# Performance work log

Hardware: AMD Instinct MI355X
Metric: run time of the kernel (lower is better)

Reference implementation:

```python
import jax, jax.numpy as jnp
import numpy as np
import math

NUM_HEADS = 16
ATTN_WIDTH = 256


def setup_inputs() -> dict:
    key = jax.random.key(0)
    ks = jax.random.split(key, 5)
    B, S, C, H = 2, 2048, 1024, 1024
    scale = 0.02
    return {
        "x": jax.random.normal(ks[0], (B, S, C), dtype=jnp.float32),
        "Wq": jax.random.normal(ks[1], (C, H), dtype=jnp.float32) * scale,
        "Wk": jax.random.normal(ks[2], (C, H), dtype=jnp.float32) * scale,
        "Wv": jax.random.normal(ks[3], (C, H), dtype=jnp.float32) * scale,
        "Wo": jax.random.normal(ks[4], (H, C), dtype=jnp.float32) * scale,
    }


def reference(x, Wq, Wk, Wv, Wo):
    B, S, C = x.shape
    H = NUM_HEADS
    dh = Wq.shape[1] // H  # head dim; Q.size(-1) in torch code

    def split_heads(t):
        # [B, S, H*dh] -> [B, H, S, dh]
        return t.reshape(B, S, H, dh).transpose(0, 2, 1, 3)

    q = split_heads(x @ Wq)
    k = split_heads(x @ Wk)
    v = split_heads(x @ Wv)

    scores = jnp.einsum("bhqd,bhkd->bhqk", q, k) / math.sqrt(dh)
    # exp-shift (first 'softmax-like' step, unnormalized)
    scores = jnp.exp(scores - jnp.max(scores, axis=-1, keepdims=True))
    # banded mask: tril(attn_width//2 - 1).triu(-(attn_width//2))
    i = jnp.arange(S)[:, None]
    j = jnp.arange(S)[None, :]
    d = j - i
    half = ATTN_WIDTH // 2
    mask = (d <= half - 1) & (d >= -half)
    scores = jnp.where(mask, scores, 0.0)
    # second softmax over the masked exp-scores (zeros contribute exp(0)=1)
    weights = jax.nn.softmax(scores, axis=-1)

    out = jnp.einsum("bhqk,bhkd->bhqd", weights, v)  # [B, H, S, dh]
    out = out.transpose(0, 2, 1, 3).reshape(B, S, H * dh)
    return out @ Wo
```

## Files before the change

### kernel.cpp

```cpp
#include <hip/hip_runtime.h>
#include <math.h>

typedef __bf16 bf16_t;
typedef bf16_t bf16x8 __attribute__((ext_vector_type(8)));
typedef bf16_t bf16x4 __attribute__((ext_vector_type(4)));
typedef float f32x4 __attribute__((ext_vector_type(4)));

constexpr int S_ = 2048;
constexpr float SCALE = 0.125f;

#define MFMA_B16(a, b, c) __builtin_amdgcn_mfma_f32_16x16x32_bf16(a, b, c, 0, 0, 0)

#define WAIT_VM0()   __builtin_amdgcn_s_waitcnt(0x0F70)
#define WAIT_LGKM0() __builtin_amdgcn_s_waitcnt(0xC07F)
#define BARRIER()    __builtin_amdgcn_s_barrier()

typedef __attribute__((address_space(1))) const void* as1_cvp;
typedef __attribute__((address_space(3))) void* as3_vp;

__device__ __forceinline__ void gl2lds16(const void* g, void* l)
{
    __builtin_amdgcn_global_load_lds((as1_cvp)g, (as3_vp)l, 16, 0, 0);
}

__global__ __launch_bounds__(256) void prep(const float* __restrict__ x,
                                            const float* __restrict__ Wq,
                                            const float* __restrict__ Wk,
                                            const float* __restrict__ Wv,
                                            const float* __restrict__ Wo,
                                            bf16_t* __restrict__ xb,
                                            bf16_t* __restrict__ Wqt,
                                            bf16_t* __restrict__ Wkt,
                                            bf16_t* __restrict__ Wvt,
                                            bf16_t* __restrict__ Wot,
                                            float* __restrict__ vsp)
{
    __shared__ float T[64][65];
    const int blk = blockIdx.x;
    const int tid = threadIdx.x;
    if (blk < 1024) {
#pragma unroll
        for (int u = 0; u < 4; ++u) {
            const int g = blk * 1024 + u * 256 + tid;
            const float4 v = ((const float4*)x)[g];
            bf16x4 o;
            o[0] = (bf16_t)v.x; o[1] = (bf16_t)v.y;
            o[2] = (bf16_t)v.z; o[3] = (bf16_t)v.w;
            *(bf16x4*)&xb[(size_t)g * 4] = o;
        }
    } else if (blk < 2048) {
        const int rem = blk - 1024;
        const int wsel = rem >> 8, t = rem & 255;
        const float* src = (wsel == 0) ? Wq : (wsel == 1) ? Wk : (wsel == 2) ? Wv : Wo;
        bf16_t* dst = (wsel == 0) ? Wqt : (wsel == 1) ? Wkt : (wsel == 2) ? Wvt : Wot;
        const int k0 = (t >> 4) * 64, n0 = (t & 15) * 64;
        const int rr = tid >> 4, c4 = (tid & 15) * 4;
#pragma unroll
        for (int u = 0; u < 4; ++u) {
            const float4 v = *(const float4*)&src[(size_t)(k0 + u * 16 + rr) * 1024 + n0 + c4];
            T[u * 16 + rr][c4 + 0] = v.x; T[u * 16 + rr][c4 + 1] = v.y;
            T[u * 16 + rr][c4 + 2] = v.z; T[u * 16 + rr][c4 + 3] = v.w;
        }
        __syncthreads();
#pragma unroll
        for (int u = 0; u < 4; ++u) {
            bf16x4 o;
#pragma unroll
            for (int e = 0; e < 4; ++e) o[e] = (bf16_t)T[c4 + e][u * 16 + rr];
            *(bf16x4*)&dst[(size_t)(n0 + u * 16 + rr) * 1024 + k0 + c4] = o;
        }
    } else {
#pragma unroll
        for (int u = 0; u < 8; ++u) vsp[u * 256 + tid] = 0.f;
    }
}

template <int MODE>
__device__ __forceinline__ void mfma_gemm_body(const bf16_t* __restrict__ A,
                                               const bf16_t* __restrict__ Bt,
                                               void* __restrict__ dst,
                                               float* __restrict__ vsum_out,
                                               int m0, int n0)
{
    __shared__ bf16_t As[8192];
    __shared__ bf16_t Bs[8192];

    const int tid = threadIdx.x;
    const int lane = tid & 63, wid = tid >> 6;
    const int l15 = lane & 15, quad = lane >> 4;
    const int wm = (wid & 1) * 64, wn = (wid >> 1) * 64;

    const int srow = wid * 32 + (lane >> 2);
    const int scg8 = (lane & 3) * 8;
    const bf16_t* Ag0 = A  + (size_t)(m0 + srow) * 1024 + scg8;
    const bf16_t* Ag1 = A  + (size_t)(m0 + srow + 16) * 1024 + scg8;
    const bf16_t* Bg0 = Bt + (size_t)(n0 + srow) * 1024 + scg8;
    const bf16_t* Bg1 = Bt + (size_t)(n0 + srow + 16) * 1024 + scg8;

    f32x4 acc[4][4];
#pragma unroll
    for (int i = 0; i < 4; ++i)
#pragma unroll
        for (int j = 0; j < 4; ++j) acc[i][j] = (f32x4){0.f, 0.f, 0.f, 0.f};

    gl2lds16(Ag0, As + (wid * 2 + 0) * 512);
    gl2lds16(Ag1, As + (wid * 2 + 1) * 512);
    gl2lds16(Bg0, Bs + (wid * 2 + 0) * 512);
    gl2lds16(Bg1, Bs + (wid * 2 + 1) * 512);

    for (int it = 0; it < 32; ++it) {
        WAIT_VM0();
        BARRIER();
        const int cur = it & 1, nxt = cur ^ 1;
        if (it + 1 < 32) {
            const int k0 = (it + 1) * 32;
            gl2lds16(Ag0 + k0, As + nxt * 4096 + (wid * 2 + 0) * 512);
            gl2lds16(Ag1 + k0, As + nxt * 4096 + (wid * 2 + 1) * 512);
            gl2lds16(Bg0 + k0, Bs + nxt * 4096 + (wid * 2 + 0) * 512);
            gl2lds16(Bg1 + k0, Bs + nxt * 4096 + (wid * 2 + 1) * 512);
        }
        bf16x8 af[4], bfr[4];
#pragma unroll
        for (int mt = 0; mt < 4; ++mt)
            af[mt] = *(const bf16x8*)&As[cur * 4096 + (wm + mt * 16 + l15) * 32 + quad * 8];
#pragma unroll
        for (int nt = 0; nt < 4; ++nt)
            bfr[nt] = *(const bf16x8*)&Bs[cur * 4096 + (wn + nt * 16 + l15) * 32 + quad * 8];
#pragma unroll
        for (int mt = 0; mt < 4; ++mt)
#pragma unroll
            for (int nt = 0; nt < 4; ++nt)
                acc[mt][nt] = MFMA_B16(bfr[nt], af[mt], acc[mt][nt]);
    }

#pragma unroll
    for (int mt = 0; mt < 4; ++mt) {
        const int m = m0 + wm + mt * 16 + l15;
#pragma unroll
        for (int nt = 0; nt < 4; ++nt) {
            const int nb = n0 + wn + nt * 16 + quad * 4;
            if (MODE == 0) {
                *(f32x4*)&((float*)dst)[(size_t)m * 1024 + nb] = acc[mt][nt];
            } else {
                const int bb = m >> 11, s = m & 2047;
                const int hh = nb >> 6, d = nb & 63;
                bf16x4 o;
#pragma unroll
                for (int u = 0; u < 4; ++u) o[u] = (bf16_t)acc[mt][nt][u];
                *(bf16x4*)&((bf16_t*)dst)[((size_t)(bb * 16 + hh) * 2048 + s) * 64 + d] = o;
            }
        }
    }

    if (MODE == 1 && vsum_out != nullptr) {
        const int bb = m0 >> 11;
#pragma unroll
        for (int nt = 0; nt < 4; ++nt) {
            f32x4 p = acc[0][nt];
#pragma unroll
            for (int mt = 1; mt < 4; ++mt) {
                p[0] += acc[mt][nt][0]; p[1] += acc[mt][nt][1];
                p[2] += acc[mt][nt][2]; p[3] += acc[mt][nt][3];
            }
#pragma unroll
            for (int st = 1; st < 16; st <<= 1) {
                p[0] += __shfl_xor(p[0], st);
                p[1] += __shfl_xor(p[1], st);
                p[2] += __shfl_xor(p[2], st);
                p[3] += __shfl_xor(p[3], st);
            }
            if (l15 == 0) {
                const int nI = n0 + wn + nt * 16 + quad * 4;
                float* vp = &vsum_out[(bb * 16 + (nI >> 6)) * 64 + (nI & 63)];
                atomicAdd(vp + 0, p[0]);
                atomicAdd(vp + 1, p[1]);
                atomicAdd(vp + 2, p[2]);
                atomicAdd(vp + 3, p[3]);
            }
        }
    }
}

__global__ __launch_bounds__(256) void gemm_qkv_mfma(const bf16_t* __restrict__ xb,
                                                     const bf16_t* __restrict__ Wqt,
                                                     const bf16_t* __restrict__ Wkt,
                                                     const bf16_t* __restrict__ Wvt,
                                                     bf16_t* Qh, bf16_t* Kh, bf16_t* Vh,
                                                     float* vsp)
{
    const bf16_t* Bt = (blockIdx.z == 0) ? Wqt : (blockIdx.z == 1) ? Wkt : Wvt;
    bf16_t* dst = (blockIdx.z == 0) ? Qh : (blockIdx.z == 1) ? Kh : Vh;
    float* vs = (blockIdx.z == 2) ? vsp : nullptr;
    mfma_gemm_body<1>(xb, Bt, dst, vs, blockIdx.y * 128, blockIdx.x * 128);
}

__global__ __launch_bounds__(256) void gemm_out_mfma(const bf16_t* __restrict__ attn,
                                                     const bf16_t* __restrict__ Wot,
                                                     float* __restrict__ out)
{
    mfma_gemm_body<0>(attn, Wot, out, nullptr, blockIdx.y * 128, blockIdx.x * 128);
}

__global__ __launch_bounds__(256, 4) void attn_fused(const bf16_t* __restrict__ Qh,
                                                     const bf16_t* __restrict__ Kh,
                                                     const bf16_t* __restrict__ Vh,
                                                     const float* __restrict__ vsp,
                                                     bf16_t* __restrict__ attn)
{
    __shared__ bf16_t pool[17920];
    __shared__ float msh[4][8][16];

    bf16_t* Ks2 = pool;
    bf16_t* Vt  = pool + 4096;
    bf16_t* Ws  = pool + 8704;
    float (*zsh)[32] = (float(*)[32])msh;

    const int tid = threadIdx.x;
    const int lane = tid & 63, wid = tid >> 6;
    const int l15 = lane & 15, quad = lane >> 4;

    const int f = blockIdx.x;
    const int seq = f >> 3;
    const int bh = (f & 7) + 8 * (seq >> 4);
    const int i0 = (seq & 15) * 128;
    const int b = bh >> 4, h = bh & 15;
    const bf16_t* Qb = Qh + (size_t)bh * 131072;
    const bf16_t* Kb = Kh + (size_t)bh * 131072;
    const bf16_t* Vb = Vh + (size_t)bh * 131072;

#pragma unroll
    for (int c = 0; c < 4; ++c) {
        const int g = wid * 4 + c;
        const int half = g >> 3;
        const int row = (g & 7) * 16 + (lane >> 2);
        gl2lds16(Qb + (size_t)(i0 + row) * 64 + half * 32 + (lane & 3) * 8,
                 pool + g * 512);
        gl2lds16(Kb + (size_t)row * 64 + half * 32 + (lane & 3) * 8,
                 pool + 8192 + g * 512);
    }
    WAIT_VM0();
    BARRIER();

    bf16x8 af[8][2];
#pragma unroll
    for (int mt = 0; mt < 8; ++mt)
#pragma unroll
        for (int ks = 0; ks < 2; ++ks)
            af[mt][ks] = *(const bf16x8*)&pool[ks * 4096 + (mt * 16 + l15) * 32 + quad * 8];
    WAIT_LGKM0();

    float rmax[8];
#pragma unroll
    for (int mt = 0; mt < 8; ++mt) rmax[mt] = -3.0e38f;

    for (int jc = 0; jc < 16; ++jc) {
        if (jc) WAIT_VM0();
        BARRIER();
        if (jc + 1 < 16) {
            bf16_t* nb = pool + (jc & 1) * 8192;
#pragma unroll
            for (int c = 0; c < 4; ++c) {
                const int g = wid * 4 + c;
                const int half = g >> 3;
                const int row = (g & 7) * 16 + (lane >> 2);
                gl2lds16(Kb + (size_t)((jc + 1) * 128 + row) * 64 + half * 32 + (lane & 3) * 8,
                         nb + g * 512);
            }
        }
        const bf16_t* cb = pool + (((jc + 1) & 1)) * 8192;
#pragma unroll
        for (int ntl = 0; ntl < 2; ++ntl) {
            const int jt = wid * 2 + ntl;
            const bf16x8 b0 = *(const bf16x8*)&cb[(jt * 16 + l15) * 32 + quad * 8];
            const bf16x8 b1 = *(const bf16x8*)&cb[4096 + (jt * 16 + l15) * 32 + quad * 8];
#pragma unroll
            for (int mt = 0; mt < 8; ++mt) {
                f32x4 t = (f32x4){0.f, 0.f, 0.f, 0.f};
                t = MFMA_B16(b0, af[mt][0], t);
                t = MFMA_B16(b1, af[mt][1], t);
                rmax[mt] = fmaxf(rmax[mt], fmaxf(fmaxf(t[0], t[1]), fmaxf(t[2], t[3])));
            }
        }
    }
#pragma unroll
    for (int mt = 0; mt < 8; ++mt) {
        float v = rmax[mt];
        v = fmaxf(v, __shfl_xor(v, 16));
        v = fmaxf(v, __shfl_xor(v, 32));
        if (quad == 0) msh[wid][mt][l15] = v;
    }
    __syncthreads();

    float mreg[2][4];
#pragma unroll
    for (int t = 0; t < 2; ++t)
#pragma unroll
        for (int r = 0; r < 4; ++r) {
            const int mt = wid * 2 + t;
            const int il = quad * 4 + r;
            mreg[t][r] = SCALE * fmaxf(fmaxf(msh[0][mt][il], msh[1][mt][il]),
                                       fmaxf(msh[2][mt][il], msh[3][mt][il]));
        }

    f32x4 vsd4[4];
#pragma unroll
    for (int dt = 0; dt < 4; ++dt)
        vsd4[dt] = *(const f32x4*)&vsp[bh * 64 + dt * 16 + quad * 4];

    f32x4 accO[2][4];
#pragma unroll
    for (int t = 0; t < 2; ++t)
#pragma unroll
        for (int dt = 0; dt < 4; ++dt) accO[t][dt] = (f32x4){0.f, 0.f, 0.f, 0.f};
    float zp[2][4] = {{0.f, 0.f, 0.f, 0.f}, {0.f, 0.f, 0.f, 0.f}};

    for (int cb2 = 0; cb2 < 6; ++cb2) {
        const int jb = i0 - 128 + cb2 * 64;
        if (jb < 0 || jb >= S_) continue;

        __syncthreads();
#pragma unroll
        for (int c = 0; c < 2; ++c) {
            const int g = wid * 2 + c;
            const int half = g >> 2;
            const int row = (g & 3) * 16 + (lane >> 2);
            gl2lds16(Kb + (size_t)(jb + row) * 64 + half * 32 + (lane & 3) * 8,
                     Ks2 + g * 512);
        }
        {
            const bf16x8 v0 = *(const bf16x8*)&Vb[(size_t)(jb + lane) * 64 + wid * 16];
            const bf16x8 v1 = *(const bf16x8*)&Vb[(size_t)(jb + lane) * 64 + wid * 16 + 8];
#pragma unroll
            for (int e = 0; e < 8; ++e) {
                Vt[(wid * 16 + e) * 72 + lane] = v0[e];
                Vt[(wid * 16 + 8 + e) * 72 + lane] = v1[e];
            }
        }
        __syncthreads();

#pragma unroll
        for (int t = 0; t < 2; ++t) {
            const int mt = wid * 2 + t;
#pragma unroll
            for (int jt4 = 0; jt4 < 4; ++jt4) {
                const bf16x8 k0 = *(const bf16x8*)&Ks2[(jt4 * 16 + l15) * 32 + quad * 8];
                const bf16x8 k1 = *(const bf16x8*)&Ks2[2048 + (jt4 * 16 + l15) * 32 + quad * 8];
                f32x4 sc = (f32x4){0.f, 0.f, 0.f, 0.f};
                sc = MFMA_B16(af[mt][0], k0, sc);
                sc = MFMA_B16(af[mt][1], k1, sc);
#pragma unroll
                for (int r = 0; r < 4; ++r) {
                    const int ig = i0 + mt * 16 + quad * 4 + r;
                    const int jg = jb + jt4 * 16 + l15;
                    const int dd = jg - ig;
                    const bool ok = (dd >= -128) && (dd <= 127);
                    const float e1 = __expf(sc[r] * SCALE - mreg[t][r]);
                    const float wv = ok ? (__expf(e1) - 1.0f) : 0.0f;
                    const bf16_t wb = (bf16_t)wv;
                    zp[t][r] += (float)wb;
                    Ws[(mt * 16 + quad * 4 + r) * 72 + jt4 * 16 + l15] = wb;
                }
            }
        }
        __syncthreads();

#pragma unroll
        for (int ks = 0; ks < 2; ++ks) {
            bf16x8 bv[4];
#pragma unroll
            for (int dt = 0; dt < 4; ++dt)
                bv[dt] = *(const bf16x8*)&Vt[(dt * 16 + l15) * 72 + ks * 32 + quad * 8];
#pragma unroll
            for (int t = 0; t < 2; ++t) {
                const int mt = wid * 2 + t;
                const bf16x8 aw = *(const bf16x8*)&Ws[(mt * 16 + l15) * 72 + ks * 32 + quad * 8];
#pragma unroll
                for (int dt = 0; dt < 4; ++dt)
                    accO[t][dt] = MFMA_B16(bv[dt], aw, accO[t][dt]);
            }
        }
    }

#pragma unroll
    for (int t = 0; t < 2; ++t)
#pragma unroll
        for (int r = 0; r < 4; ++r) {
            float z = zp[t][r];
            z += __shfl_xor(z, 1);
            z += __shfl_xor(z, 2);
            z += __shfl_xor(z, 4);
            z += __shfl_xor(z, 8);
            if (l15 == 0) zsh[wid][t * 16 + quad * 4 + r] = z + (float)S_;
        }
    __syncthreads();

#pragma unroll
    for (int t = 0; t < 2; ++t) {
        const float rz = 1.0f / zsh[wid][t * 16 + l15];
        const int irow = i0 + (wid * 2 + t) * 16 + l15;
#pragma unroll
        for (int dt = 0; dt < 4; ++dt) {
            bf16x4 o;
#pragma unroll
            for (int r = 0; r < 4; ++r)
                o[r] = (bf16_t)((accO[t][dt][r] + vsd4[dt][r]) * rz);
            *(bf16x4*)&attn[(size_t)(b * S_ + irow) * 1024 + h * 64 + dt * 16 + quad * 4] = o;
        }
    }
}

extern "C" void kernel_launch(void* const* d_in, const int* in_sizes, int n_in,
                              void* d_out, int out_size, void* d_ws, size_t ws_size,
                              hipStream_t stream)
{
    const float* x  = (const float*)d_in[0];
    const float* Wq = (const float*)d_in[1];
    const float* Wk = (const float*)d_in[2];
    const float* Wv = (const float*)d_in[3];
    const float* Wo = (const float*)d_in[4];
    float* out = (float*)d_out;

    char* ws = (char*)d_ws;
    bf16_t* xb   = (bf16_t*)(ws + 0);
    bf16_t* Wqt  = (bf16_t*)(ws + 8388608);
    bf16_t* Wkt  = (bf16_t*)(ws + 10485760);
    bf16_t* Wvt  = (bf16_t*)(ws + 12582912);
    bf16_t* Wot  = (bf16_t*)(ws + 14680064);
    bf16_t* Qh   = (bf16_t*)(ws + 16777216);
    bf16_t* Kh   = (bf16_t*)(ws + 25165824);
    bf16_t* Vh   = (bf16_t*)(ws + 33554432);
    bf16_t* attn = (bf16_t*)(ws + 41943040);
    float*  vsp  = (float*)(ws + 50331648);

    prep<<<2049, 256, 0, stream>>>(x, Wq, Wk, Wv, Wo, xb, Wqt, Wkt, Wvt, Wot, vsp);
    gemm_qkv_mfma<<<dim3(8, 32, 3), 256, 0, stream>>>(xb, Wqt, Wkt, Wvt, Qh, Kh, Vh, vsp);
    attn_fused<<<512, 256, 0, stream>>>(Qh, Kh, Vh, vsp, attn);
    gemm_out_mfma<<<dim3(8, 32), 256, 0, stream>>>(attn, Wot, out);
}
```

Measured before the change: 208.9 us.

## Triple-buffer LDS global loads in GEMM and attention max-pass loops

Replaces double buffering with a three-stage ring of LDS buffers in the shared GEMM body and in the attention kernel's K max-scan loop. Loads are issued two iterations ahead, and partial vmcnt waits (4 or 8 outstanding) replace full drains. The attention kernel also gets a separate Q buffer, so the first K tiles can stream while Q fragments load. The cost is more LDS per block: GEMM LDS grows by half, and attention drops its occupancy hint of 4 blocks, which may reduce the number of resident blocks.

```diff
diff --git a/kernel.cpp b/kernel.cpp
--- a/kernel.cpp
+++ b/kernel.cpp
@@ -11,9 +11,10 @@
 
 #define MFMA_B16(a, b, c) __builtin_amdgcn_mfma_f32_16x16x32_bf16(a, b, c, 0, 0, 0)
 
-#define WAIT_VM0()   __builtin_amdgcn_s_waitcnt(0x0F70)
-#define WAIT_LGKM0() __builtin_amdgcn_s_waitcnt(0xC07F)
-#define BARRIER()    __builtin_amdgcn_s_barrier()
+#define WAIT_VM0() __builtin_amdgcn_s_waitcnt(0x0F70)
+#define WAIT_VM4() __builtin_amdgcn_s_waitcnt(0x0F74)
+#define WAIT_VM8() __builtin_amdgcn_s_waitcnt(0x0F78)
+#define BARRIER()  __builtin_amdgcn_s_barrier()
 
 typedef __attribute__((address_space(1))) const void* as1_cvp;
 typedef __attribute__((address_space(3))) void* as3_vp;
@@ -82,8 +83,8 @@
                                                float* __restrict__ vsum_out,
                                                int m0, int n0)
 {
-    __shared__ bf16_t As[8192];
-    __shared__ bf16_t Bs[8192];
+    __shared__ bf16_t As[12288];
+    __shared__ bf16_t Bs[12288];
 
     const int tid = threadIdx.x;
     const int lane = tid & 63, wid = tid >> 6;
@@ -103,34 +104,40 @@
 #pragma unroll
         for (int j = 0; j < 4; ++j) acc[i][j] = (f32x4){0.f, 0.f, 0.f, 0.f};
 
-    gl2lds16(Ag0, As + (wid * 2 + 0) * 512);
-    gl2lds16(Ag1, As + (wid * 2 + 1) * 512);
-    gl2lds16(Bg0, Bs + (wid * 2 + 0) * 512);
-    gl2lds16(Bg1, Bs + (wid * 2 + 1) * 512);
-
+#pragma unroll
+    for (int p = 0; p < 2; ++p) {
+        const int k0 = p * 32;
+        gl2lds16(Ag0 + k0, As + p * 4096 + (wid * 2 + 0) * 512);
+        gl2lds16(Ag1 + k0, As + p * 4096 + (wid * 2 + 1) * 512);
+        gl2lds16(Bg0 + k0, Bs + p * 4096 + (wid * 2 + 0) * 512);
+        gl2lds16(Bg1 + k0, Bs + p * 4096 + (wid * 2 + 1) * 512);
+    }
+
+    int cbuf = 0, sbuf = 2;
     for (int it = 0; it < 32; ++it) {
-        WAIT_VM0();
+        if (it + 2 < 32) WAIT_VM4(); else WAIT_VM0();
         BARRIER();
-        const int cur = it & 1, nxt = cur ^ 1;
-        if (it + 1 < 32) {
-            const int k0 = (it + 1) * 32;
-            gl2lds16(Ag0 + k0, As + nxt * 4096 + (wid * 2 + 0) * 512);
-            gl2lds16(Ag1 + k0, As + nxt * 4096 + (wid * 2 + 1) * 512);
-            gl2lds16(Bg0 + k0, Bs + nxt * 4096 + (wid * 2 + 0) * 512);
-            gl2lds16(Bg1 + k0, Bs + nxt * 4096 + (wid * 2 + 1) * 512);
+        if (it + 2 < 32) {
+            const int k0 = (it + 2) * 32;
+            gl2lds16(Ag0 + k0, As + sbuf * 4096 + (wid * 2 + 0) * 512);
+            gl2lds16(Ag1 + k0, As + sbuf * 4096 + (wid * 2 + 1) * 512);
+            gl2lds16(Bg0 + k0, Bs + sbuf * 4096 + (wid * 2 + 0) * 512);
+            gl2lds16(Bg1 + k0, Bs + sbuf * 4096 + (wid * 2 + 1) * 512);
+            sbuf = (sbuf == 2) ? 0 : sbuf + 1;
         }
         bf16x8 af[4], bfr[4];
 #pragma unroll
         for (int mt = 0; mt < 4; ++mt)
-            af[mt] = *(const bf16x8*)&As[cur * 4096 + (wm + mt * 16 + l15) * 32 + quad * 8];
+            af[mt] = *(const bf16x8*)&As[cbuf * 4096 + (wm + mt * 16 + l15) * 32 + quad * 8];
 #pragma unroll
         for (int nt = 0; nt < 4; ++nt)
-            bfr[nt] = *(const bf16x8*)&Bs[cur * 4096 + (wn + nt * 16 + l15) * 32 + quad * 8];
+            bfr[nt] = *(const bf16x8*)&Bs[cbuf * 4096 + (wn + nt * 16 + l15) * 32 + quad * 8];
 #pragma unroll
         for (int mt = 0; mt < 4; ++mt)
 #pragma unroll
             for (int nt = 0; nt < 4; ++nt)
                 acc[mt][nt] = MFMA_B16(bfr[nt], af[mt], acc[mt][nt]);
+        cbuf = (cbuf == 2) ? 0 : cbuf + 1;
     }
 
 #pragma unroll
@@ -201,19 +208,20 @@
     mfma_gemm_body<0>(attn, Wot, out, nullptr, blockIdx.y * 128, blockIdx.x * 128);
 }
 
-__global__ __launch_bounds__(256, 4) void attn_fused(const bf16_t* __restrict__ Qh,
-                                                     const bf16_t* __restrict__ Kh,
-                                                     const bf16_t* __restrict__ Vh,
-                                                     const float* __restrict__ vsp,
-                                                     bf16_t* __restrict__ attn)
-{
-    __shared__ bf16_t pool[17920];
+__global__ __launch_bounds__(256) void attn_fused(const bf16_t* __restrict__ Qh,
+                                                  const bf16_t* __restrict__ Kh,
+                                                  const bf16_t* __restrict__ Vh,
+                                                  const float* __restrict__ vsp,
+                                                  bf16_t* __restrict__ attn)
+{
+    __shared__ bf16_t Qs[8192];
+    __shared__ bf16_t Kp[24576];
     __shared__ float msh[4][8][16];
-
-    bf16_t* Ks2 = pool;
-    bf16_t* Vt  = pool + 4096;
-    bf16_t* Ws  = pool + 8704;
     float (*zsh)[32] = (float(*)[32])msh;
+
+    bf16_t* Ks2 = Kp;
+    bf16_t* Vt  = Kp + 4096;
+    bf16_t* Ws  = Kp + 8704;
 
     const int tid = threadIdx.x;
     const int lane = tid & 63, wid = tid >> 6;
@@ -234,11 +242,20 @@
         const int half = g >> 3;
         const int row = (g & 7) * 16 + (lane >> 2);
         gl2lds16(Qb + (size_t)(i0 + row) * 64 + half * 32 + (lane & 3) * 8,
-                 pool + g * 512);
-        gl2lds16(Kb + (size_t)row * 64 + half * 32 + (lane & 3) * 8,
-                 pool + 8192 + g * 512);
-    }
-    WAIT_VM0();
+                 Qs + g * 512);
+    }
+#pragma unroll
+    for (int p = 0; p < 2; ++p) {
+#pragma unroll
+        for (int c = 0; c < 4; ++c) {
+            const int g = wid * 4 + c;
+            const int half = g >> 3;
+            const int row = (g & 7) * 16 + (lane >> 2);
+            gl2lds16(Kb + (size_t)(p * 128 + row) * 64 + half * 32 + (lane & 3) * 8,
+                     Kp + p * 8192 + g * 512);
+        }
+    }
+    WAIT_VM8();
     BARRIER();
 
     bf16x8 af[8][2];
@@ -246,28 +263,29 @@
     for (int mt = 0; mt < 8; ++mt)
 #pragma unroll
         for (int ks = 0; ks < 2; ++ks)
-            af[mt][ks] = *(const bf16x8*)&pool[ks * 4096 + (mt * 16 + l15) * 32 + quad * 8];
-    WAIT_LGKM0();
+            af[mt][ks] = *(const bf16x8*)&Qs[ks * 4096 + (mt * 16 + l15) * 32 + quad * 8];
 
     float rmax[8];
 #pragma unroll
     for (int mt = 0; mt < 8; ++mt) rmax[mt] = -3.0e38f;
 
+    int cbuf = 0, sbuf = 2;
     for (int jc = 0; jc < 16; ++jc) {
-        if (jc) WAIT_VM0();
+        if (jc + 2 < 16) WAIT_VM4(); else WAIT_VM0();
         BARRIER();
-        if (jc + 1 < 16) {
-            bf16_t* nb = pool + (jc & 1) * 8192;
+        if (jc + 2 < 16) {
+            bf16_t* nb = Kp + sbuf * 8192;
 #pragma unroll
             for (int c = 0; c < 4; ++c) {
                 const int g = wid * 4 + c;
                 const int half = g >> 3;
                 const int row = (g & 7) * 16 + (lane >> 2);
-                gl2lds16(Kb + (size_t)((jc + 1) * 128 + row) * 64 + half * 32 + (lane & 3) * 8,
+                gl2lds16(Kb + (size_t)((jc + 2) * 128 + row) * 64 + half * 32 + (lane & 3) * 8,
                          nb + g * 512);
             }
-        }
-        const bf16_t* cb = pool + (((jc + 1) & 1)) * 8192;
+            sbuf = (sbuf == 2) ? 0 : sbuf + 1;
+        }
+        const bf16_t* cb = Kp + cbuf * 8192;
 #pragma unroll
         for (int ntl = 0; ntl < 2; ++ntl) {
             const int jt = wid * 2 + ntl;
@@ -281,6 +299,7 @@
                 rmax[mt] = fmaxf(rmax[mt], fmaxf(fmaxf(t[0], t[1]), fmaxf(t[2], t[3])));
             }
         }
+        cbuf = (cbuf == 2) ? 0 : cbuf + 1;
     }
 #pragma unroll
     for (int mt = 0; mt < 8; ++mt) {
```

Measured after the change: 190.0 us. 9.1% less time.
